# Kernel optimization log

Measured on AMD Instinct MI355X. Metric: run time of the kernel, lower is better.

## Reference

```python
import jax, jax.numpy as jnp
import numpy as np


def _conv3x3(x, w):
    # NCHW input, OIHW weight, stride 1, padding 1 (SAME for 3x3)
    return jax.lax.conv_general_dilated(
        x, w, window_strides=(1, 1), padding=((1, 1), (1, 1)),
        dimension_numbers=('NCHW', 'OIHW', 'NCHW'))


def _conv1x1(x, w):
    return jax.lax.conv_general_dilated(
        x, w, window_strides=(1, 1), padding=((0, 0), (0, 0)),
        dimension_numbers=('NCHW', 'OIHW', 'NCHW'))


def setup_inputs() -> dict:
    key = jax.random.key(0)
    k_x, k_w1, k_w2, k_wm = jax.random.split(key, 4)
    N, C, H, W = 16, 256, 64, 64
    fan = C * 9
    x = jax.random.normal(k_x, (N, C, H, W), dtype=jnp.float32)
    w1 = jax.random.normal(k_w1, (C, C, 3, 3), dtype=jnp.float32) * (2.0 / fan) ** 0.5
    w2 = jax.random.normal(k_w2, (C, C, 3, 3), dtype=jnp.float32) * (2.0 / fan) ** 0.5
    w_mask = jax.random.normal(k_wm, (1, C, 1, 1), dtype=jnp.float32) * (1.0 / C) ** 0.5
    b_mask = jnp.zeros((1,), dtype=jnp.float32)
    return {'x': x, 'w1': w1, 'w2': w2, 'w_mask': w_mask, 'b_mask': b_mask}


def reference(x, w1, w2, w_mask, b_mask):
    # MaskUnit: 1x1 conv -> logits -> hard binary mask (straight-through estimator)
    logits = _conv1x1(x, w_mask) + b_mask[None, :, None, None]  # [N,1,H,W]
    hard = (logits > 0).astype(x.dtype)
    mask = logits + jax.lax.stop_gradient(hard - logits)        # std mask, binary in fwd
    # dilated mask: 3x3 max-pool (covers 3x3 receptive field of active outputs)
    mask_dilate = jax.lax.reduce_window(
        mask, -jnp.inf, jax.lax.max, (1, 1, 3, 3), (1, 1, 1, 1), 'SAME')
    # sparse branch: conv1 gated by dilated mask, conv2 gated by std mask
    h = jax.nn.relu(_conv3x3(x, w1) * mask_dilate)
    h = jax.nn.relu(_conv3x3(h, w2) * mask)
    # apply_mask + residual (mask binary -> h*mask == h already, kept for fidelity)
    out = x + h * mask
    return out
```

## Files before the change

### kernel.cpp

```cpp
#include <hip/hip_runtime.h>
#include <hip/hip_bf16.h>

#define C_ 256
#define H_ 64
#define W_ 64
#define N_ 16
#define HW_ 4096
#define IMG_ (C_ * HW_)
#define PADIMG_ (66 * 66 * 256)
#define WT_ELEMS_ (9 * 16 * 256 * 16)

typedef short bf16x8 __attribute__((ext_vector_type(8)));
typedef float f32x16 __attribute__((ext_vector_type(16)));

__device__ __forceinline__ unsigned short f2bf(float f) {
  __hip_bfloat16 h = __float2bfloat16(f);
  return *reinterpret_cast<unsigned short*>(&h);
}

__device__ __forceinline__ void gld_lds16(const void* g, void* l) {
  __builtin_amdgcn_global_load_lds(
      (const __attribute__((address_space(1))) void*)g,
      (__attribute__((address_space(3))) void*)l, 16, 0, 0);
}

__global__ __launch_bounds__(256) void xpadmask_kernel(
    const float* __restrict__ x, const float* __restrict__ wm,
    const float* __restrict__ bm, short* __restrict__ Xp,
    unsigned char* __restrict__ mask) {
  __shared__ unsigned short lds[64 * 260];
  __shared__ float wms[256];
  __shared__ double sums[4][64];
  const int h = blockIdx.x, img = blockIdx.y;
  const int tid = threadIdx.x;
  const int wv = tid >> 6, wl = tid & 63;
  wms[tid] = wm[tid];
  __syncthreads();
  const float* xi = x + (size_t)img * IMG_ + h * 64;
  double a0 = 0.0, a1 = 0.0, a2 = 0.0, a3 = 0.0;
#pragma unroll 4
  for (int i = 0; i < 16; ++i) {
#pragma unroll
    for (int u = 0; u < 4; ++u) {
      int c = (i * 4 + u) * 4 + wv;
      float v = xi[(size_t)c * HW_ + wl];
      lds[wl * 260 + c] = f2bf(v);
      double p = (double)v * (double)wms[c];
      if (u == 0) a0 += p;
      else if (u == 1) a1 += p;
      else if (u == 2) a2 += p;
      else a3 += p;
    }
  }
  sums[wv][wl] = (a0 + a1) + (a2 + a3);
  __syncthreads();
  short* Xpi = Xp + (size_t)img * PADIMG_ + ((h + 1) * 66 + 1) * 256;
#pragma unroll
  for (int j = 0; j < 16; ++j) {
    int w = j * 4 + wv;
    int c4 = wl * 4;
    uint2 d = *(const uint2*)&lds[w * 260 + c4];
    *(uint2*)&Xpi[(size_t)w * 256 + c4] = d;
  }
  if (wv == 0) {
    double t = sums[0][wl] + sums[1][wl] + sums[2][wl] + sums[3][wl] +
               (double)bm[0];
    mask[img * HW_ + h * 64 + wl] = (t > 0.0) ? 1 : 0;
  }
}

__global__ __launch_bounds__(256) void wt_kernel(
    const float* __restrict__ w1, const float* __restrict__ w2,
    short* __restrict__ Wt1, short* __restrict__ Wt2) {
  const int k = blockIdx.x, c = threadIdx.x;
  const float* src = blockIdx.y ? w2 : w1;
  short* dst = blockIdx.y ? Wt2 : Wt1;
  const float* s = src + ((size_t)k * 256 + c) * 9;
  const int kc = c >> 4, ce = c & 15;
#pragma unroll
  for (int t = 0; t < 9; ++t)
    dst[(((size_t)t * 16 + kc) * 256 + k) * 16 + ce] = (short)f2bf(s[t]);
}

__global__ __launch_bounds__(128) void halo_zero(short* __restrict__ Xp,
                                                 short* __restrict__ Hp) {
  int p = blockIdx.x;
  int r, c;
  if (p < 66) { r = 0; c = p; }
  else if (p < 132) { r = 65; c = p - 66; }
  else if (p < 196) { r = p - 131; c = 0; }
  else { r = p - 195; c = 65; }
  short* buf = blockIdx.z ? Hp : Xp;
  unsigned int* d = (unsigned int*)(buf + (size_t)blockIdx.y * PADIMG_ +
                                    (size_t)(r * 66 + c) * 256);
  d[threadIdx.x] = 0u;
}

#define BBUF 10560

__device__ __forceinline__ void stage_B(short* sm, int buf, const short* Xb,
                                        int ko, int wave, int lane) {
  short* Bd = sm + buf * BBUF;
#pragma unroll
  for (int q = 0; q < 6; ++q) {
    int n = wave + 4 * q;
    if (n > 21) n = 21;
    const int h = (n >= 11) ? 1 : 0;
    const int i = n - h * 11;
    const int row0 = (i < 10) ? i * 64 : 596;
    gld_lds16(Xb + (size_t)(row0 + lane) * 256 + ko + h * 8,
              Bd + h * 5280 + row0 * 8);
  }
}

template <int EPI>
__global__ __launch_bounds__(256, 2) void conv_mfma(
    const short* __restrict__ src, const short* __restrict__ Wt,
    const unsigned char* __restrict__ gate, const float* __restrict__ xres,
    short* __restrict__ dstH, float* __restrict__ dstF, int swz) {
  __shared__ __align__(16) short sm[3 * BBUF];

  const int tid = threadIdx.x;
  const int lane = tid & 63, wave = tid >> 6;
  const int ln31 = lane & 31, kh = lane >> 5;

  int bx, by, bz;
  {
    int d = blockIdx.x + 4 * (blockIdx.y + 8 * blockIdx.z);
    if (swz) {
      int k = d & 7, j = d >> 3;
      bx = j & 3;
      by = (j >> 2) & 7;
      bz = ((j >> 5) << 3) + k;
    } else {
      bx = blockIdx.x;
      by = blockIdx.y;
      bz = blockIdx.z;
    }
  }
  const int ch0 = bx * 64;
  const int h0 = by * 8;
  const int img = bz;

  const short* Xb = src + (size_t)img * PADIMG_ + (size_t)(h0 * 66) * 256;
  const short* WL = Wt + ((size_t)(ch0 + ln31)) * 16 + kh * 8;

  f32x16 acc[2][4];
#pragma unroll
  for (int i = 0; i < 2; ++i)
#pragma unroll
    for (int j = 0; j < 4; ++j)
#pragma unroll
      for (int e = 0; e < 16; ++e) acc[i][j][e] = 0.f;

  stage_B(sm, 0, Xb, 0, wave, lane);
  stage_B(sm, 1, Xb, 16, wave, lane);
  bf16x8 wc0 = *(const bf16x8*)(WL);
  bf16x8 wc1 = *(const bf16x8*)(WL + 512);
  bf16x8 wn0 = *(const bf16x8*)(WL + 16 * 4096);
  bf16x8 wn1 = *(const bf16x8*)(WL + 16 * 4096 + 512);
  asm volatile("s_waitcnt vmcnt(4)\n\ts_barrier" ::: "memory");

  int c0 = 0, c1 = 1, c2 = 2;
  for (int kk = 0; kk < 16; ++kk) {
    const short* Bth = sm + c0 * BBUF + kh * 5280 + (wave * 132 + ln31) * 8;
    bf16x8 bc[4], bn[4];
#pragma unroll
    for (int j = 0; j < 4; ++j)
      bc[j] = *(const bf16x8*)(Bth + ((j >> 1) * 66 + (j & 1) * 32) * 8);
#pragma unroll
    for (int t = 0; t < 9; ++t) {
      const int nt = t + 2;
      const int ntkc = (nt < 9) ? (nt * 16 + kk) : ((nt - 9) * 16 + kk + 1);
      bf16x8 f0 = *(const bf16x8*)(WL + (size_t)ntkc * 4096);
      bf16x8 f1 = *(const bf16x8*)(WL + (size_t)ntkc * 4096 + 512);
      if (t < 8) {
        const int dy = (t + 1) / 3, dx = (t + 1) % 3;
#pragma unroll
        for (int j = 0; j < 4; ++j)
          bn[j] = *(const bf16x8*)(Bth +
                                   (((j >> 1) + dy) * 66 + (j & 1) * 32 + dx) * 8);
      }
      __builtin_amdgcn_s_setprio(1);
#pragma unroll
      for (int j = 0; j < 4; ++j) {
        acc[0][j] = __builtin_amdgcn_mfma_f32_32x32x16_bf16(wc0, bc[j],
                                                            acc[0][j], 0, 0, 0);
        acc[1][j] = __builtin_amdgcn_mfma_f32_32x32x16_bf16(wc1, bc[j],
                                                            acc[1][j], 0, 0, 0);
      }
      __builtin_amdgcn_s_setprio(0);
      wc0 = wn0; wc1 = wn1; wn0 = f0; wn1 = f1;
      if (t < 8) {
#pragma unroll
        for (int j = 0; j < 4; ++j) bc[j] = bn[j];
      }
    }
    if (kk < 14) stage_B(sm, c2, Xb, (kk + 2) * 16, wave, lane);
    if (kk < 15) asm volatile("s_barrier" ::: "memory");
    const int tmp = c0;
    c0 = c1;
    c1 = c2;
    c2 = tmp;
  }

  const int rb = h0 + wave * 2;
#pragma unroll
  for (int j = 0; j < 4; ++j) {
    const int r = rb + (j >> 1);
    const int col = (j & 1) * 32 + ln31;
    const int pidx = r * 64 + col;
    unsigned int g;
    if (EPI == 0) {
      g = 0;
#pragma unroll
      for (int dy = -1; dy <= 1; ++dy) {
        const int rr = r + dy;
        if (rr < 0 || rr >= H_) continue;
#pragma unroll
        for (int dx = -1; dx <= 1; ++dx) {
          const int cc = col + dx;
          if (cc < 0 || cc >= W_) continue;
          g |= gate[img * HW_ + rr * W_ + cc];
        }
      }
    } else {
      g = gate[img * HW_ + pidx];
    }
#pragma unroll
    for (int i = 0; i < 2; ++i) {
      const f32x16 v = acc[i][j];
#pragma unroll
      for (int rg = 0; rg < 4; ++rg) {
        const int ch = ch0 + i * 32 + rg * 8 + kh * 4;
        float e0 = g ? fmaxf(v[rg * 4 + 0], 0.f) : 0.f;
        float e1 = g ? fmaxf(v[rg * 4 + 1], 0.f) : 0.f;
        float e2 = g ? fmaxf(v[rg * 4 + 2], 0.f) : 0.f;
        float e3 = g ? fmaxf(v[rg * 4 + 3], 0.f) : 0.f;
        if (EPI == 0) {
          uint2 u;
          u.x = (unsigned int)f2bf(e0) | ((unsigned int)f2bf(e1) << 16);
          u.y = (unsigned int)f2bf(e2) | ((unsigned int)f2bf(e3) << 16);
          short* dp = dstH + (size_t)img * PADIMG_ +
                      ((size_t)((r + 1) * 66 + (col + 1))) * 256 + ch;
          *(uint2*)dp = u;
        } else {
          size_t o = (size_t)img * IMG_ + (size_t)ch * HW_ + pidx;
          dstF[o] = xres[o] + e0;
          dstF[o + HW_] = xres[o + HW_] + e1;
          dstF[o + 2 * HW_] = xres[o + 2 * HW_] + e2;
          dstF[o + 3 * HW_] = xres[o + 3 * HW_] + e3;
        }
      }
    }
  }
}

extern "C" void kernel_launch(void* const* d_in, const int* in_sizes, int n_in,
                              void* d_out, int out_size, void* d_ws,
                              size_t ws_size, hipStream_t stream) {
  const float* x = (const float*)d_in[0];
  const float* w1 = (const float*)d_in[1];
  const float* w2 = (const float*)d_in[2];
  const float* wmask = (const float*)d_in[3];
  const float* bmask = (const float*)d_in[4];
  float* out = (float*)d_out;

  char* ws = (char*)d_ws;
  unsigned char* mask = (unsigned char*)ws;
  short* Wt1 = (short*)(ws + 65536);
  short* Wt2 = Wt1 + WT_ELEMS_;
  const size_t fixed = 65536 + 4 * (size_t)WT_ELEMS_;
  short* Xp = (short*)(ws + fixed);

  const size_t tailpad = 32768;
  const size_t per_img = 2 * (size_t)PADIMG_ * 2;
  int B = (ws_size > fixed + tailpad)
              ? (int)((ws_size - fixed - tailpad) / per_img) : 0;
  if (B > N_) B = N_;
  if (B < 1) B = 1;
  short* Hp = Xp + (size_t)B * PADIMG_;

  wt_kernel<<<dim3(256, 2), 256, 0, stream>>>(w1, w2, Wt1, Wt2);
  halo_zero<<<dim3(260, B, 2), 128, 0, stream>>>(Xp, Hp);

  for (int n0 = 0; n0 < N_; n0 += B) {
    const int nb = (N_ - n0 < B) ? (N_ - n0) : B;
    const int swz = (nb % 8 == 0) ? 1 : 0;
    xpadmask_kernel<<<dim3(64, nb), 256, 0, stream>>>(
        x + (size_t)n0 * IMG_, wmask, bmask, Xp, mask + n0 * HW_);
    conv_mfma<0><<<dim3(4, 8, nb), 256, 0, stream>>>(
        Xp, Wt1, mask + n0 * HW_, nullptr, Hp, nullptr, swz);
    conv_mfma<1><<<dim3(4, 8, nb), 256, 0, stream>>>(
        Hp, Wt2, mask + n0 * HW_, x + (size_t)n0 * IMG_, nullptr,
        out + (size_t)n0 * IMG_, swz);
  }
}
```

Measured before the change: 300.2 us.

## Split conv tile across eight waves with one output row each, drop register prefetch

The conv kernel now launches 512 threads (8 waves) per block instead of 256, so each wave covers one output row (2 column tiles) instead of two rows, halving the accumulators per wave. The software prefetch of next-tap B fragments and two-ahead weight fragments is removed in favour of loading B per tap, and LDS staging is spread over eight waves. The aim is to cut register pressure and raise occupancy (launch bounds 512,4) so latency is hidden by more waves. In exchange, each weight fragment is reused by fewer MFMAs, so more global weight loads per FLOP and less explicit overlap within a wave.

```diff
diff --git a/kernel.cpp b/kernel.cpp
--- a/kernel.cpp
+++ b/kernel.cpp
@@ -102,8 +102,8 @@
                                         int ko, int wave, int lane) {
   short* Bd = sm + buf * BBUF;
 #pragma unroll
-  for (int q = 0; q < 6; ++q) {
-    int n = wave + 4 * q;
+  for (int q = 0; q < 3; ++q) {
+    int n = wave + 8 * q;
     if (n > 21) n = 21;
     const int h = (n >= 11) ? 1 : 0;
     const int i = n - h * 11;
@@ -114,7 +114,7 @@
 }
 
 template <int EPI>
-__global__ __launch_bounds__(256, 2) void conv_mfma(
+__global__ __launch_bounds__(512, 4) void conv_mfma(
     const short* __restrict__ src, const short* __restrict__ Wt,
     const unsigned char* __restrict__ gate, const float* __restrict__ xres,
     short* __restrict__ dstH, float* __restrict__ dstF, int swz) {
@@ -145,11 +145,11 @@
   const short* Xb = src + (size_t)img * PADIMG_ + (size_t)(h0 * 66) * 256;
   const short* WL = Wt + ((size_t)(ch0 + ln31)) * 16 + kh * 8;
 
-  f32x16 acc[2][4];
+  f32x16 acc[2][2];
 #pragma unroll
   for (int i = 0; i < 2; ++i)
 #pragma unroll
-    for (int j = 0; j < 4; ++j)
+    for (int j = 0; j < 2; ++j)
 #pragma unroll
       for (int e = 0; e < 16; ++e) acc[i][j][e] = 0.f;
 
@@ -157,44 +157,32 @@
   stage_B(sm, 1, Xb, 16, wave, lane);
   bf16x8 wc0 = *(const bf16x8*)(WL);
   bf16x8 wc1 = *(const bf16x8*)(WL + 512);
-  bf16x8 wn0 = *(const bf16x8*)(WL + 16 * 4096);
-  bf16x8 wn1 = *(const bf16x8*)(WL + 16 * 4096 + 512);
-  asm volatile("s_waitcnt vmcnt(4)\n\ts_barrier" ::: "memory");
+  asm volatile("s_waitcnt vmcnt(2)\n\ts_barrier" ::: "memory");
 
   int c0 = 0, c1 = 1, c2 = 2;
   for (int kk = 0; kk < 16; ++kk) {
-    const short* Bth = sm + c0 * BBUF + kh * 5280 + (wave * 132 + ln31) * 8;
-    bf16x8 bc[4], bn[4];
-#pragma unroll
-    for (int j = 0; j < 4; ++j)
-      bc[j] = *(const bf16x8*)(Bth + ((j >> 1) * 66 + (j & 1) * 32) * 8);
+    const short* Bth = sm + c0 * BBUF + kh * 5280 + (wave * 66 + ln31) * 8;
 #pragma unroll
     for (int t = 0; t < 9; ++t) {
-      const int nt = t + 2;
-      const int ntkc = (nt < 9) ? (nt * 16 + kk) : ((nt - 9) * 16 + kk + 1);
-      bf16x8 f0 = *(const bf16x8*)(WL + (size_t)ntkc * 4096);
-      bf16x8 f1 = *(const bf16x8*)(WL + (size_t)ntkc * 4096 + 512);
-      if (t < 8) {
-        const int dy = (t + 1) / 3, dx = (t + 1) % 3;
-#pragma unroll
-        for (int j = 0; j < 4; ++j)
-          bn[j] = *(const bf16x8*)(Bth +
-                                   (((j >> 1) + dy) * 66 + (j & 1) * 32 + dx) * 8);
-      }
+      const int ntkc = (t < 8) ? ((t + 1) * 16 + kk) : (kk + 1);
+      bf16x8 na0 = *(const bf16x8*)(WL + (size_t)ntkc * 4096);
+      bf16x8 na1 = *(const bf16x8*)(WL + (size_t)ntkc * 4096 + 512);
+      const int dy = t / 3, dx = t % 3;
+      bf16x8 b[2];
+#pragma unroll
+      for (int j = 0; j < 2; ++j)
+        b[j] = *(const bf16x8*)(Bth + (dy * 66 + j * 32 + dx) * 8);
       __builtin_amdgcn_s_setprio(1);
 #pragma unroll
-      for (int j = 0; j < 4; ++j) {
-        acc[0][j] = __builtin_amdgcn_mfma_f32_32x32x16_bf16(wc0, bc[j],
+      for (int j = 0; j < 2; ++j) {
+        acc[0][j] = __builtin_amdgcn_mfma_f32_32x32x16_bf16(wc0, b[j],
                                                             acc[0][j], 0, 0, 0);
-        acc[1][j] = __builtin_amdgcn_mfma_f32_32x32x16_bf16(wc1, bc[j],
+        acc[1][j] = __builtin_amdgcn_mfma_f32_32x32x16_bf16(wc1, b[j],
                                                             acc[1][j], 0, 0, 0);
       }
       __builtin_amdgcn_s_setprio(0);
-      wc0 = wn0; wc1 = wn1; wn0 = f0; wn1 = f1;
-      if (t < 8) {
-#pragma unroll
-        for (int j = 0; j < 4; ++j) bc[j] = bn[j];
-      }
+      wc0 = na0;
+      wc1 = na1;
     }
     if (kk < 14) stage_B(sm, c2, Xb, (kk + 2) * 16, wave, lane);
     if (kk < 15) asm volatile("s_barrier" ::: "memory");
@@ -204,11 +192,10 @@
     c2 = tmp;
   }
 
-  const int rb = h0 + wave * 2;
-#pragma unroll
-  for (int j = 0; j < 4; ++j) {
-    const int r = rb + (j >> 1);
-    const int col = (j & 1) * 32 + ln31;
+  const int r = h0 + wave;
+#pragma unroll
+  for (int j = 0; j < 2; ++j) {
+    const int col = j * 32 + ln31;
     const int pidx = r * 64 + col;
     unsigned int g;
     if (EPI == 0) {
@@ -289,9 +276,9 @@
     const int swz = (nb % 8 == 0) ? 1 : 0;
     xpadmask_kernel<<<dim3(64, nb), 256, 0, stream>>>(
         x + (size_t)n0 * IMG_, wmask, bmask, Xp, mask + n0 * HW_);
-    conv_mfma<0><<<dim3(4, 8, nb), 256, 0, stream>>>(
+    conv_mfma<0><<<dim3(4, 8, nb), 512, 0, stream>>>(
         Xp, Wt1, mask + n0 * HW_, nullptr, Hp, nullptr, swz);
-    conv_mfma<1><<<dim3(4, 8, nb), 256, 0, stream>>>(
+    conv_mfma<1><<<dim3(4, 8, nb), 512, 0, stream>>>(
         Hp, Wt2, mask + n0 * HW_, x + (size_t)n0 * IMG_, nullptr,
         out + (size_t)n0 * IMG_, swz);
   }
```

New measurement: 314.6 us. 1.05x slower.
